# Performance work log

Hardware: AMD Instinct MI355X
Metric: run time of the kernel (lower is better)

The kernel has to match this reference:

```python
import jax, jax.numpy as jnp
import numpy as np

D = 1024  # encoder_output_size

def setup_inputs() -> dict:
    key = jax.random.key(0)
    ks = jax.random.split(key, 5)
    scale = 1.0 / np.sqrt(D)  # roughly matches nn.Linear init spread
    seq = jax.random.normal(ks[0], (2048, 8, D), dtype=jnp.float32)
    Kw1 = jax.random.normal(ks[1], (D, D), dtype=jnp.float32) * scale
    Kw2 = jax.random.normal(ks[2], (D, D), dtype=jnp.float32) * scale
    Qw1 = jax.random.normal(ks[3], (D, D), dtype=jnp.float32) * scale
    Qw2 = jax.random.normal(ks[4], (D, D), dtype=jnp.float32) * scale
    return {"sequence": seq, "Kw1": Kw1, "Kw2": Kw2, "Qw1": Qw1, "Qw2": Qw2}

def _mlp(x, W1, W2):
    # nn.Linear(bias=False): y = x @ W^T ; tanh after each
    return jnp.tanh(jnp.tanh(x @ W1.T) @ W2.T)

def reference(sequence, Kw1, Kw2, Qw1, Qw2):
    x = jnp.transpose(sequence, (1, 0, 2))          # [B, S, D]
    keys = _mlp(x, Kw1, Kw2)                        # [B, S, D]
    queries = _mlp(x, Qw1, Qw2)                     # [B, S, D]
    scale = 1.0 / jnp.sqrt(jnp.float32(x.shape[-1]))
    weights = jnp.einsum('bsd,btd->bst', keys, queries) * scale  # [B, S, S]
    weights = jax.nn.softmax(weights, axis=-1)
    attended = jnp.einsum('bst,btd->bsd', weights, x)            # [B, S, D]
    return jnp.transpose(attended, (1, 0, 2))       # [S, B, D]
```

## Files before the change

### kernel.cpp

```cpp
#include <hip/hip_runtime.h>
#include <hip/hip_bf16.h>

#define SEQ 2048
#define NB 8
#define DIM 1024

typedef __attribute__((ext_vector_type(4))) float f32x4;
typedef __attribute__((ext_vector_type(8))) short bf16x8;
typedef __attribute__((ext_vector_type(4))) unsigned short u16x4;

__device__ __forceinline__ unsigned short f2bf(float f) {
    __hip_bfloat16 h = __float2bfloat16(f);
    return *reinterpret_cast<unsigned short*>(&h);
}
__device__ __forceinline__ float bf2f(unsigned short u) {
    union { unsigned u; float f; } x; x.u = ((unsigned)u) << 16;
    return x.f;
}
__device__ __forceinline__ float fast_tanh(float x) {
    float e = __expf(x + x);
    float r = __builtin_amdgcn_rcpf(e + 1.0f);
    return fmaf(-2.0f, r, 1.0f);
}

__global__ __launch_bounds__(256) void convert_w4(const float* __restrict__ kw1,
                                                  const float* __restrict__ kw2,
                                                  const float* __restrict__ qw1,
                                                  const float* __restrict__ qw2,
                                                  unsigned short* __restrict__ out) {
    int sel = blockIdx.y;
    const float* src = sel == 0 ? kw1 : (sel == 1 ? qw1 : (sel == 2 ? kw2 : qw2));
    int i = blockIdx.x * 256 + threadIdx.x;
    float4 v = reinterpret_cast<const float4*>(src)[i];
    u16x4 o = { f2bf(v.x), f2bf(v.y), f2bf(v.z), f2bf(v.w) };
    reinterpret_cast<u16x4*>(out + (size_t)sel * DIM * DIM)[i] = o;
}

__global__ __launch_bounds__(256) void make_xbxbT(const float* __restrict__ seq,
                                                  unsigned short* __restrict__ xb,
                                                  unsigned short* __restrict__ xbT) {
    __shared__ unsigned short tile[64][65];
    int s0 = blockIdx.x * 64, d0 = blockIdx.y * 64, b = blockIdx.z;
    int t = threadIdx.x;
    int dx = (t & 15) * 4, sy = t >> 4;
    #pragma unroll
    for (int i = 0; i < 4; ++i) {
        int s = s0 + sy + i * 16;
        float4 v = *reinterpret_cast<const float4*>(seq + ((size_t)s * NB + b) * DIM + d0 + dx);
        u16x4 o = { f2bf(v.x), f2bf(v.y), f2bf(v.z), f2bf(v.w) };
        tile[sy + i * 16][dx + 0] = o[0];
        tile[sy + i * 16][dx + 1] = o[1];
        tile[sy + i * 16][dx + 2] = o[2];
        tile[sy + i * 16][dx + 3] = o[3];
        *reinterpret_cast<u16x4*>(xb + ((size_t)b * SEQ + s) * DIM + d0 + dx) = o;
    }
    __syncthreads();
    int sx = (t & 15) * 4, dy = t >> 4;
    #pragma unroll
    for (int i = 0; i < 4; ++i) {
        int d = d0 + dy + i * 16;
        u16x4 o = { tile[sx + 0][dy + i * 16], tile[sx + 1][dy + i * 16],
                    tile[sx + 2][dy + i * 16], tile[sx + 3][dy + i * 16] };
        *reinterpret_cast<u16x4*>(xbT + ((size_t)b * DIM + d) * SEQ + s0 + sx) = o;
    }
}

__device__ __forceinline__ void gload16(const unsigned short* g, unsigned short* l) {
    __builtin_amdgcn_global_load_lds((const __attribute__((address_space(1))) void*)g,
                                     (__attribute__((address_space(3))) void*)l,
                                     16, 0, 0);
}

#define MFMA16(I0, J0)                                                                            \
    _Pragma("unroll")                                                                             \
    for (int ks = 0; ks < 2; ++ks)                                                                \
        _Pragma("unroll")                                                                         \
        for (int ii = 0; ii < 4; ++ii)                                                            \
            _Pragma("unroll")                                                                     \
            for (int jj = 0; jj < 2; ++jj)                                                        \
                acc[I0 + ii][J0 + jj] = __builtin_amdgcn_mfma_f32_16x16x32_bf16(                   \
                    a[I0 + ii][ks], b[J0 + jj][ks], acc[I0 + ii][J0 + jj], 0, 0, 0);

template<int MODE>
__global__ __launch_bounds__(512, 2) void gemm256(
    const unsigned short* __restrict__ A, size_t sA, int lda,
    const unsigned short* __restrict__ B, size_t sB, int ldb,
    void* __restrict__ Cv, size_t sC, int ldc,
    int K, float scale, float* __restrict__ rowsum)
{
    __shared__ unsigned short AsF[2 * 2 * 8192];
    __shared__ unsigned short BsF[2 * 2 * 8192];

    const int gx = gridDim.x, gy = gridDim.y;
    const int nwg = gx * gy * gridDim.z;
    const int fid = blockIdx.x + gx * (blockIdx.y + gy * blockIdx.z);
    const int cpx = nwg >> 3;
    const int sw = (fid & 7) * cpx + (fid >> 3);
    const int bx = sw % gx;
    const int rem = sw / gx;
    const int by = rem % gy;
    const int bz = rem / gy;

    const unsigned short* Ab = A + sA * bz;
    const unsigned short* Bb = B + sB * bz;
    const int m0 = by * 256;
    const int n0 = bx * 256;

    const int t_ = threadIdx.x;
    const int lane = t_ & 63;
    const int w = t_ >> 6;
    const int wm = w >> 2;
    const int wn = w & 3;

    if (MODE == 0 && rowsum != nullptr && bx == 0 && bz == 0 && t_ < 256)
        rowsum[m0 + t_] = 0.0f;

    const int l3 = lane >> 3;
    const int g7 = lane & 7;
    const size_t h128a = (size_t)128 * lda, r8a = (size_t)8 * lda;
    const size_t h128b = (size_t)128 * ldb, r8b = (size_t)8 * ldb;
    const unsigned short* gA = Ab + (size_t)(m0 + w * 16 + l3) * lda + ((g7 ^ l3) << 3);
    const unsigned short* gB = Bb + (size_t)(n0 + w * 16 + l3) * ldb + ((g7 ^ l3) << 3);

    const int fr = lane & 15;
    const int hi4 = lane >> 4;
    const int off0 = fr * 64 + (((hi4) ^ g7) << 3);
    const int off1 = fr * 64 + (((4 + hi4) ^ g7) << 3);
    const int bno = (wn & 1) * 4096;
    const int wlds = w * 1024;

    f32x4 acc[8][4] = {};
    const int NT = K >> 6;

    gload16(gA, AsF + wlds);                     gload16(gA + r8a, AsF + wlds + 512);
    gload16(gA + h128a, AsF + 8192 + wlds);      gload16(gA + h128a + r8a, AsF + 8192 + wlds + 512);
    gload16(gB, BsF + wlds);                     gload16(gB + r8b, BsF + wlds + 512);
    gload16(gB + h128b, BsF + 8192 + wlds);      gload16(gB + h128b + r8b, BsF + 8192 + wlds + 512);
    {
        const unsigned short* gb1 = gB + 64;
        gload16(gb1, BsF + 16384 + wlds);                gload16(gb1 + r8b, BsF + 16384 + wlds + 512);
        gload16(gb1 + h128b, BsF + 16384 + 8192 + wlds); gload16(gb1 + h128b + r8b, BsF + 16384 + 8192 + wlds + 512);
    }
    asm volatile("s_waitcnt vmcnt(4)" ::: "memory");
    __builtin_amdgcn_s_barrier();

    const unsigned short* gA1 = gA + 64;
    const unsigned short* gB2 = gB + 128;

    for (int u = 0; u < NT; ++u) {
        const int bu = (u & 1) * 16384;
        const int bn = 16384 - bu;
        const unsigned short* pA = AsF + bu + wm * 8192;
        const unsigned short* pB = BsF + bu + (wn >> 1) * 8192 + bno;
        const bool pfA = (u + 1 < NT);
        const bool pfB = (u + 2 < NT);
        bf16x8 a[8][2], b[4][2];

        #pragma unroll
        for (int i = 0; i < 4; ++i) {
            a[i][0] = *(const bf16x8*)&pA[i * 1024 + off0];
            a[i][1] = *(const bf16x8*)&pA[i * 1024 + off1];
        }
        #pragma unroll
        for (int j = 0; j < 2; ++j) {
            b[j][0] = *(const bf16x8*)&pB[j * 1024 + off0];
            b[j][1] = *(const bf16x8*)&pB[j * 1024 + off1];
        }
        if (pfA) { gload16(gA1, AsF + bn + wlds); gload16(gA1 + r8a, AsF + bn + wlds + 512); }
        asm volatile("s_waitcnt lgkmcnt(8)" ::: "memory");
        __builtin_amdgcn_s_barrier();
        asm volatile("s_waitcnt lgkmcnt(0)" ::: "memory");
        __builtin_amdgcn_sched_barrier(0);
        __builtin_amdgcn_s_setprio(1);
        MFMA16(0, 0)
        __builtin_amdgcn_s_setprio(0);
        __builtin_amdgcn_s_barrier();

        #pragma unroll
        for (int j = 2; j < 4; ++j) {
            b[j][0] = *(const bf16x8*)&pB[j * 1024 + off0];
            b[j][1] = *(const bf16x8*)&pB[j * 1024 + off1];
        }
        if (pfA) { gload16(gA1 + h128a, AsF + bn + 8192 + wlds); gload16(gA1 + h128a + r8a, AsF + bn + 8192 + wlds + 512); }
        __builtin_amdgcn_s_barrier();
        asm volatile("s_waitcnt lgkmcnt(0)" ::: "memory");
        __builtin_amdgcn_sched_barrier(0);
        __builtin_amdgcn_s_setprio(1);
        MFMA16(0, 2)
        __builtin_amdgcn_s_setprio(0);
        __builtin_amdgcn_s_barrier();

        #pragma unroll
        for (int i = 4; i < 8; ++i) {
            a[i][0] = *(const bf16x8*)&pA[i * 1024 + off0];
            a[i][1] = *(const bf16x8*)&pA[i * 1024 + off1];
        }
        if (pfB) { gload16(gB2, BsF + bu + wlds); gload16(gB2 + r8b, BsF + bu + wlds + 512); }
        __builtin_amdgcn_s_barrier();
        asm volatile("s_waitcnt lgkmcnt(0)" ::: "memory");
        __builtin_amdgcn_sched_barrier(0);
        __builtin_amdgcn_s_setprio(1);
        MFMA16(4, 0)
        __builtin_amdgcn_s_setprio(0);
        __builtin_amdgcn_s_barrier();

        if (pfB) {
            gload16(gB2 + h128b, BsF + bu + 8192 + wlds);
            gload16(gB2 + h128b + r8b, BsF + bu + 8192 + wlds + 512);
            asm volatile("s_waitcnt vmcnt(4)" ::: "memory");
        } else {
            asm volatile("s_waitcnt vmcnt(0)" ::: "memory");
        }
        __builtin_amdgcn_s_barrier();
        __builtin_amdgcn_sched_barrier(0);
        __builtin_amdgcn_s_setprio(1);
        MFMA16(4, 2)
        __builtin_amdgcn_s_setprio(0);
        __builtin_amdgcn_s_barrier();

        gA1 += 64; gB2 += 64;
    }

    if (MODE == 0) {
        unsigned short* C = reinterpret_cast<unsigned short*>(Cv) + sC * bz;
        #pragma unroll
        for (int mi = 0; mi < 8; ++mi)
            #pragma unroll
            for (int ni = 0; ni < 4; ++ni)
                #pragma unroll
                for (int r = 0; r < 4; ++r) {
                    int row = m0 + wm * 128 + mi * 16 + hi4 * 4 + r;
                    int col = n0 + wn * 64 + ni * 16 + fr;
                    C[(size_t)row * ldc + col] = f2bf(fast_tanh(acc[mi][ni][r]));
                }
    } else if (MODE == 3) {
        unsigned short* C = reinterpret_cast<unsigned short*>(Cv) + sC * bz;
        #pragma unroll
        for (int mi = 0; mi < 8; ++mi)
            #pragma unroll
            for (int r = 0; r < 4; ++r) {
                int row = m0 + wm * 128 + mi * 16 + hi4 * 4 + r;
                float ps = 0.f;
                #pragma unroll
                for (int ni = 0; ni < 4; ++ni) {
                    unsigned short h = f2bf(__expf(acc[mi][ni][r] * scale));
                    C[(size_t)row * ldc + (n0 + wn * 64 + ni * 16 + fr)] = h;
                    ps += bf2f(h);
                }
                ps += __shfl_xor(ps, 1, 64);
                ps += __shfl_xor(ps, 2, 64);
                ps += __shfl_xor(ps, 4, 64);
                ps += __shfl_xor(ps, 8, 64);
                if (fr == 0) atomicAdd(&rowsum[(size_t)bz * SEQ + row], ps);
            }
    } else {
        float* C = reinterpret_cast<float*>(Cv) + sC * bz;
        #pragma unroll
        for (int mi = 0; mi < 8; ++mi)
            #pragma unroll
            for (int r = 0; r < 4; ++r) {
                int row = m0 + wm * 128 + mi * 16 + hi4 * 4 + r;
                float invs = 1.0f / rowsum[(size_t)bz * SEQ + row];
                #pragma unroll
                for (int ni = 0; ni < 4; ++ni) {
                    int col = n0 + wn * 64 + ni * 16 + fr;
                    C[(size_t)row * ldc + col] = acc[mi][ni][r] * invs;
                }
            }
    }
}

extern "C" void kernel_launch(void* const* d_in, const int* in_sizes, int n_in,
                              void* d_out, int out_size, void* d_ws, size_t ws_size,
                              hipStream_t stream) {
    const float* seq  = (const float*)d_in[0];
    const float* Kw1f = (const float*)d_in[1];
    const float* Kw2f = (const float*)d_in[2];
    const float* Qw1f = (const float*)d_in[3];
    const float* Qw2f = (const float*)d_in[4];
    float* out = (float*)d_out;

    char* ws = (char*)d_ws;
    const size_t MB = 1024 * 1024;
    unsigned short* W    = (unsigned short*)(ws);
    unsigned short* Wkq1 = W;
    unsigned short* Wk2s = W + 2 * (size_t)DIM * DIM;
    unsigned short* xbT  = (unsigned short*)(ws + 8 * MB);
    unsigned short* hKQ  = (unsigned short*)(ws + 40 * MB);
    unsigned short* kq   = (unsigned short*)(ws + 104 * MB);
    unsigned short* xb   = kq;
    unsigned short* P    = hKQ;
    float* rowsum        = (float*)(ws);

    convert_w4<<<dim3(DIM * DIM / 4 / 256, 4), 256, 0, stream>>>(Kw1f, Kw2f, Qw1f, Qw2f, W);
    make_xbxbT<<<dim3(SEQ / 64, DIM / 64, NB), 256, 0, stream>>>(seq, xb, xbT);

    gemm256<0><<<dim3(2 * DIM / 256, (NB * SEQ) / 256, 1), 512, 0, stream>>>(
        xb, 0, DIM, Wkq1, 0, DIM, hKQ, 0, 2 * DIM, DIM, 1.0f, nullptr);

    gemm256<0><<<dim3(DIM / 256, (NB * SEQ) / 256, 2), 512, 0, stream>>>(
        hKQ, (size_t)DIM, 2 * DIM, Wk2s, (size_t)DIM * DIM, DIM,
        kq, (size_t)NB * SEQ * DIM, DIM, DIM, 1.0f, rowsum);

    gemm256<3><<<dim3(SEQ / 256, SEQ / 256, NB), 512, 0, stream>>>(
        kq, (size_t)SEQ * DIM, DIM, kq + (size_t)NB * SEQ * DIM, (size_t)SEQ * DIM, DIM,
        P, (size_t)SEQ * SEQ, SEQ, DIM, 0.03125f, rowsum);

    gemm256<4><<<dim3(DIM / 256, SEQ / 256, NB), 512, 0, stream>>>(
        P, (size_t)SEQ * SEQ, SEQ, xbT, (size_t)DIM * SEQ, SEQ,
        out, (size_t)DIM, NB * DIM, SEQ, 1.0f, rowsum);
}
```

Measured before the change: 321.9 us.

## Double GEMM workgroup to 16 waves with 64x64 per-wave tiles

```diff
diff --git a/kernel.cpp b/kernel.cpp
--- a/kernel.cpp
+++ b/kernel.cpp
@@ -71,18 +71,8 @@
                                      16, 0, 0);
 }
 
-#define MFMA16(I0, J0)                                                                            \
-    _Pragma("unroll")                                                                             \
-    for (int ks = 0; ks < 2; ++ks)                                                                \
-        _Pragma("unroll")                                                                         \
-        for (int ii = 0; ii < 4; ++ii)                                                            \
-            _Pragma("unroll")                                                                     \
-            for (int jj = 0; jj < 2; ++jj)                                                        \
-                acc[I0 + ii][J0 + jj] = __builtin_amdgcn_mfma_f32_16x16x32_bf16(                   \
-                    a[I0 + ii][ks], b[J0 + jj][ks], acc[I0 + ii][J0 + jj], 0, 0, 0);
-
 template<int MODE>
-__global__ __launch_bounds__(512, 2) void gemm256(
+__global__ __launch_bounds__(1024, 4) void gemm256(
     const unsigned short* __restrict__ A, size_t sA, int lda,
     const unsigned short* __restrict__ B, size_t sB, int ldb,
     void* __restrict__ Cv, size_t sC, int ldc,
@@ -115,33 +105,27 @@
     if (MODE == 0 && rowsum != nullptr && bx == 0 && bz == 0 && t_ < 256)
         rowsum[m0 + t_] = 0.0f;
 
-    const int l3 = lane >> 3;
-    const int g7 = lane & 7;
-    const size_t h128a = (size_t)128 * lda, r8a = (size_t)8 * lda;
-    const size_t h128b = (size_t)128 * ldb, r8b = (size_t)8 * ldb;
-    const unsigned short* gA = Ab + (size_t)(m0 + w * 16 + l3) * lda + ((g7 ^ l3) << 3);
-    const unsigned short* gB = Bb + (size_t)(n0 + w * 16 + l3) * ldb + ((g7 ^ l3) << 3);
+    const int sr = t_ >> 3;
+    const int sg = t_ & 7;
+    const size_t h128a = (size_t)128 * lda;
+    const size_t h128b = (size_t)128 * ldb;
+    const unsigned short* gA = Ab + (size_t)(m0 + sr) * lda + ((sg ^ (sr & 7)) << 3);
+    const unsigned short* gB = Bb + (size_t)(n0 + sr) * ldb + ((sg ^ (sr & 7)) << 3);
+    const int tl = t_ * 8;
 
     const int fr = lane & 15;
     const int hi4 = lane >> 4;
+    const int g7 = lane & 7;
     const int off0 = fr * 64 + (((hi4) ^ g7) << 3);
     const int off1 = fr * 64 + (((4 + hi4) ^ g7) << 3);
-    const int bno = (wn & 1) * 4096;
-    const int wlds = w * 1024;
-
-    f32x4 acc[8][4] = {};
+
+    f32x4 acc[4][4] = {};
     const int NT = K >> 6;
 
-    gload16(gA, AsF + wlds);                     gload16(gA + r8a, AsF + wlds + 512);
-    gload16(gA + h128a, AsF + 8192 + wlds);      gload16(gA + h128a + r8a, AsF + 8192 + wlds + 512);
-    gload16(gB, BsF + wlds);                     gload16(gB + r8b, BsF + wlds + 512);
-    gload16(gB + h128b, BsF + 8192 + wlds);      gload16(gB + h128b + r8b, BsF + 8192 + wlds + 512);
-    {
-        const unsigned short* gb1 = gB + 64;
-        gload16(gb1, BsF + 16384 + wlds);                gload16(gb1 + r8b, BsF + 16384 + wlds + 512);
-        gload16(gb1 + h128b, BsF + 16384 + 8192 + wlds); gload16(gb1 + h128b + r8b, BsF + 16384 + 8192 + wlds + 512);
-    }
-    asm volatile("s_waitcnt vmcnt(4)" ::: "memory");
+    gload16(gA, AsF + tl);                gload16(gA + h128a, AsF + 8192 + tl);
+    gload16(gB, BsF + tl);                gload16(gB + h128b, BsF + 8192 + tl);
+    gload16(gB + 64, BsF + 16384 + tl);   gload16(gB + 64 + h128b, BsF + 16384 + 8192 + tl);
+    asm volatile("s_waitcnt vmcnt(2)" ::: "memory");
     __builtin_amdgcn_s_barrier();
 
     const unsigned short* gA1 = gA + 64;
@@ -150,29 +134,30 @@
     for (int u = 0; u < NT; ++u) {
         const int bu = (u & 1) * 16384;
         const int bn = 16384 - bu;
-        const unsigned short* pA = AsF + bu + wm * 8192;
-        const unsigned short* pB = BsF + bu + (wn >> 1) * 8192 + bno;
+        const unsigned short* pA = AsF + bu + (wm >> 1) * 8192 + (wm & 1) * 4096;
+        const unsigned short* pB = BsF + bu + (wn >> 1) * 8192 + (wn & 1) * 4096;
         const bool pfA = (u + 1 < NT);
         const bool pfB = (u + 2 < NT);
-        bf16x8 a[8][2], b[4][2];
-
-        #pragma unroll
-        for (int i = 0; i < 4; ++i) {
-            a[i][0] = *(const bf16x8*)&pA[i * 1024 + off0];
-            a[i][1] = *(const bf16x8*)&pA[i * 1024 + off1];
-        }
+        bf16x8 a[4], b[4][2];
+
+        #pragma unroll
+        for (int i = 0; i < 4; ++i) a[i] = *(const bf16x8*)&pA[i * 1024 + off0];
         #pragma unroll
         for (int j = 0; j < 2; ++j) {
             b[j][0] = *(const bf16x8*)&pB[j * 1024 + off0];
             b[j][1] = *(const bf16x8*)&pB[j * 1024 + off1];
         }
-        if (pfA) { gload16(gA1, AsF + bn + wlds); gload16(gA1 + r8a, AsF + bn + wlds + 512); }
-        asm volatile("s_waitcnt lgkmcnt(8)" ::: "memory");
+        if (pfA) gload16(gA1, AsF + bn + tl);
+        asm volatile("s_waitcnt lgkmcnt(4)" ::: "memory");
         __builtin_amdgcn_s_barrier();
         asm volatile("s_waitcnt lgkmcnt(0)" ::: "memory");
         __builtin_amdgcn_sched_barrier(0);
         __builtin_amdgcn_s_setprio(1);
-        MFMA16(0, 0)
+        #pragma unroll
+        for (int i = 0; i < 4; ++i) {
+            acc[i][0] = __builtin_amdgcn_mfma_f32_16x16x32_bf16(a[i], b[0][0], acc[i][0], 0, 0, 0);
+            acc[i][1] = __builtin_amdgcn_mfma_f32_16x16x32_bf16(a[i], b[1][0], acc[i][1], 0, 0, 0);
+        }
         __builtin_amdgcn_s_setprio(0);
         __builtin_amdgcn_s_barrier();
 
@@ -181,40 +166,48 @@
             b[j][0] = *(const bf16x8*)&pB[j * 1024 + off0];
             b[j][1] = *(const bf16x8*)&pB[j * 1024 + off1];
         }
-        if (pfA) { gload16(gA1 + h128a, AsF + bn + 8192 + wlds); gload16(gA1 + h128a + r8a, AsF + bn + 8192 + wlds + 512); }
+        if (pfA) gload16(gA1 + h128a, AsF + bn + 8192 + tl);
         __builtin_amdgcn_s_barrier();
         asm volatile("s_waitcnt lgkmcnt(0)" ::: "memory");
         __builtin_amdgcn_sched_barrier(0);
         __builtin_amdgcn_s_setprio(1);
-        MFMA16(0, 2)
+        #pragma unroll
+        for (int i = 0; i < 4; ++i) {
+            acc[i][2] = __builtin_amdgcn_mfma_f32_16x16x32_bf16(a[i], b[2][0], acc[i][2], 0, 0, 0);
+            acc[i][3] = __builtin_amdgcn_mfma_f32_16x16x32_bf16(a[i], b[3][0], acc[i][3], 0, 0, 0);
+        }
         __builtin_amdgcn_s_setprio(0);
         __builtin_amdgcn_s_barrier();
 
         #pragma unroll
-        for (int i = 4; i < 8; ++i) {
-            a[i][0] = *(const bf16x8*)&pA[i * 1024 + off0];
-            a[i][1] = *(const bf16x8*)&pA[i * 1024 + off1];
-        }
-        if (pfB) { gload16(gB2, BsF + bu + wlds); gload16(gB2 + r8b, BsF + bu + wlds + 512); }
+        for (int i = 0; i < 4; ++i) a[i] = *(const bf16x8*)&pA[i * 1024 + off1];
+        if (pfB) gload16(gB2, BsF + bu + tl);
         __builtin_amdgcn_s_barrier();
         asm volatile("s_waitcnt lgkmcnt(0)" ::: "memory");
         __builtin_amdgcn_sched_barrier(0);
         __builtin_amdgcn_s_setprio(1);
-        MFMA16(4, 0)
+        #pragma unroll
+        for (int i = 0; i < 4; ++i) {
+            acc[i][0] = __builtin_amdgcn_mfma_f32_16x16x32_bf16(a[i], b[0][1], acc[i][0], 0, 0, 0);
+            acc[i][1] = __builtin_amdgcn_mfma_f32_16x16x32_bf16(a[i], b[1][1], acc[i][1], 0, 0, 0);
+        }
         __builtin_amdgcn_s_setprio(0);
         __builtin_amdgcn_s_barrier();
 
         if (pfB) {
-            gload16(gB2 + h128b, BsF + bu + 8192 + wlds);
-            gload16(gB2 + h128b + r8b, BsF + bu + 8192 + wlds + 512);
-            asm volatile("s_waitcnt vmcnt(4)" ::: "memory");
+            gload16(gB2 + h128b, BsF + bu + 8192 + tl);
+            asm volatile("s_waitcnt vmcnt(2)" ::: "memory");
         } else {
             asm volatile("s_waitcnt vmcnt(0)" ::: "memory");
         }
         __builtin_amdgcn_s_barrier();
         __builtin_amdgcn_sched_barrier(0);
         __builtin_amdgcn_s_setprio(1);
-        MFMA16(4, 2)
+        #pragma unroll
+        for (int i = 0; i < 4; ++i) {
+            acc[i][2] = __builtin_amdgcn_mfma_f32_16x16x32_bf16(a[i], b[2][1], acc[i][2], 0, 0, 0);
+            acc[i][3] = __builtin_amdgcn_mfma_f32_16x16x32_bf16(a[i], b[3][1], acc[i][3], 0, 0, 0);
+        }
         __builtin_amdgcn_s_setprio(0);
         __builtin_amdgcn_s_barrier();
 
@@ -224,22 +217,22 @@
     if (MODE == 0) {
         unsigned short* C = reinterpret_cast<unsigned short*>(Cv) + sC * bz;
         #pragma unroll
-        for (int mi = 0; mi < 8; ++mi)
+        for (int mi = 0; mi < 4; ++mi)
             #pragma unroll
             for (int ni = 0; ni < 4; ++ni)
                 #pragma unroll
                 for (int r = 0; r < 4; ++r) {
-                    int row = m0 + wm * 128 + mi * 16 + hi4 * 4 + r;
+                    int row = m0 + wm * 64 + mi * 16 + hi4 * 4 + r;
                     int col = n0 + wn * 64 + ni * 16 + fr;
                     C[(size_t)row * ldc + col] = f2bf(fast_tanh(acc[mi][ni][r]));
                 }
     } else if (MODE == 3) {
         unsigned short* C = reinterpret_cast<unsigned short*>(Cv) + sC * bz;
         #pragma unroll
-        for (int mi = 0; mi < 8; ++mi)
+        for (int mi = 0; mi < 4; ++mi)
             #pragma unroll
             for (int r = 0; r < 4; ++r) {
-                int row = m0 + wm * 128 + mi * 16 + hi4 * 4 + r;
+                int row = m0 + wm * 64 + mi * 16 + hi4 * 4 + r;
                 float ps = 0.f;
                 #pragma unroll
                 for (int ni = 0; ni < 4; ++ni) {
@@ -256,10 +249,10 @@
     } else {
         float* C = reinterpret_cast<float*>(Cv) + sC * bz;
         #pragma unroll
-        for (int mi = 0; mi < 8; ++mi)
+        for (int mi = 0; mi < 4; ++mi)
             #pragma unroll
             for (int r = 0; r < 4; ++r) {
-                int row = m0 + wm * 128 + mi * 16 + hi4 * 4 + r;
+                int row = m0 + wm * 64 + mi * 16 + hi4 * 4 + r;
                 float invs = 1.0f / rowsum[(size_t)bz * SEQ + row];
                 #pragma unroll
                 for (int ni = 0; ni < 4; ++ni) {
@@ -295,18 +288,18 @@
     convert_w4<<<dim3(DIM * DIM / 4 / 256, 4), 256, 0, stream>>>(Kw1f, Kw2f, Qw1f, Qw2f, W);
     make_xbxbT<<<dim3(SEQ / 64, DIM / 64, NB), 256, 0, stream>>>(seq, xb, xbT);
 
-    gemm256<0><<<dim3(2 * DIM / 256, (NB * SEQ) / 256, 1), 512, 0, stream>>>(
+    gemm256<0><<<dim3(2 * DIM / 256, (NB * SEQ) / 256, 1), 1024, 0, stream>>>(
         xb, 0, DIM, Wkq1, 0, DIM, hKQ, 0, 2 * DIM, DIM, 1.0f, nullptr);
 
-    gemm256<0><<<dim3(DIM / 256, (NB * SEQ) / 256, 2), 512, 0, stream>>>(
+    gemm256<0><<<dim3(DIM / 256, (NB * SEQ) / 256, 2), 1024, 0, stream>>>(
         hKQ, (size_t)DIM, 2 * DIM, Wk2s, (size_t)DIM * DIM, DIM,
         kq, (size_t)NB * SEQ * DIM, DIM, DIM, 1.0f, rowsum);
 
-    gemm256<3><<<dim3(SEQ / 256, SEQ / 256, NB), 512, 0, stream>>>(
+    gemm256<3><<<dim3(SEQ / 256, SEQ / 256, NB), 1024, 0, stream>>>(
         kq, (size_t)SEQ * DIM, DIM, kq + (size_t)NB * SEQ * DIM, (size_t)SEQ * DIM, DIM,
         P, (size_t)SEQ * SEQ, SEQ, DIM, 0.03125f, rowsum);
 
-    gemm256<4><<<dim3(DIM / 256, SEQ / 256, NB), 512, 0, stream>>>(
+    gemm256<4><<<dim3(DIM / 256, SEQ / 256, NB), 1024, 0, stream>>>(
         P, (size_t)SEQ * SEQ, SEQ, xbT, (size_t)DIM * SEQ, SEQ,
         out, (size_t)DIM, NB * DIM, SEQ, 1.0f, rowsum);
 }
```

After: 323.9 us. No clear change (+0.6%).
